# Optimization experiments

Hardware: AMD Instinct MI355X
Metric: run time of the kernel (lower is better)

## Reference

```python
import math
import jax, jax.numpy as jnp
import numpy as np

B, N, H, NH, DD, L = 4, 384, 256, 8, 32, 4
HD = H // NH
V = 11           # num_species + 1 (padding row 0)
CUTOFF = 5.0

def _ln(x, g, b):
    m = jnp.mean(x, axis=-1, keepdims=True)
    v = jnp.mean(jnp.square(x - m), axis=-1, keepdims=True)
    return (x - m) / jnp.sqrt(v + 1e-5) * g + b

def setup_inputs() -> dict:
    key = jax.random.key(0)
    ks = iter(jax.random.split(key, 64))
    def nrm(shape, s=0.05):
        return jax.random.normal(next(ks), shape, jnp.float32) * s
    return {
        'node_indices': jax.random.randint(next(ks), (B, N), 0, V),
        'positions': jax.random.normal(next(ks), (B, N, 3), jnp.float32),
        'mask': jnp.ones((B, N), jnp.float32),
        'emb': nrm((V, H)).at[0].set(0.0),
        'ln1_g': jnp.ones((L, H)), 'ln1_b': jnp.zeros((L, H)),
        'qkv_w': nrm((L, H, 3 * H)), 'qkv_b': jnp.zeros((L, 3 * H)),
        'out_w': nrm((L, H, H)), 'out_b': jnp.zeros((L, H)),
        'rb_w1': nrm((L, DD, H)), 'rb_b1': jnp.zeros((L, H)),
        'rb_w2': nrm((L, H, NH)), 'rb_b2': jnp.zeros((L, NH)),
        'gate_w1': nrm((L, H, H)), 'gate_b1': jnp.zeros((L, H)),
        'gate_w2': nrm((L, H, H)), 'gate_b2': jnp.zeros((L, H)),
        'ln2_g': jnp.ones((L, H)), 'ln2_b': jnp.zeros((L, H)),
        'ff_w1': nrm((L, H, 2 * H)), 'ff_b1': jnp.zeros((L, 2 * H)),
        'ff_w2': nrm((L, 2 * H, H)), 'ff_b2': jnp.zeros((L, H)),
        'pool_g': jnp.ones((H,)), 'pool_beta': jnp.zeros((H,)),
        'pool_w': nrm((H, H)), 'pool_b': jnp.zeros((H,)),
        'eh_w': nrm((H, 1)), 'eh_b': jnp.zeros((1,)),
    }

def _forward(node_indices, positions, mask, emb, ln1_g, ln1_b, qkv_w, qkv_b,
             out_w, out_b, rb_w1, rb_b1, rb_w2, rb_b2, gate_w1, gate_b1,
             gate_w2, gate_b2, ln2_g, ln2_b, ff_w1, ff_b1, ff_w2, ff_b2,
             pool_g, pool_beta, pool_w, pool_b, eh_w, eh_b):
    mask_b = mask > 0
    x = emb[node_indices] * mask_b[..., None]               # [B,N,H]
    pos = positions * mask_b[..., None].astype(positions.dtype)
    rel = pos[:, :, None, :] - pos[:, None, :, :]           # [B,N,N,3]
    dist = jnp.linalg.norm(rel + 1e-9, axis=-1)             # [B,N,N]
    adj = (dist <= CUTOFF).astype(jnp.float32)
    adj = adj * mask_b[:, None, :] * mask_b[:, :, None]
    edge = adj > 0
    isolated = mask_b & ~edge.any(axis=-1)
    adj = adj + isolated.astype(jnp.float32)[:, :, None] * jnp.eye(N, dtype=jnp.float32)
    edge = adj > 0
    # Bessel envelope features [B,N,N,DD]
    kk = jnp.arange(1, DD + 1, dtype=jnp.float32)
    ang = math.pi * kk * (dist / CUTOFF)[..., None]
    feat = jnp.sin(ang) / (dist[..., None] + 1e-6)
    feat = feat * (dist <= CUTOFF)[..., None].astype(jnp.float32)
    feat = feat * adj[..., None]

    scale = math.sqrt(HD)
    NEG = jnp.finfo(jnp.float32).min
    for l in range(L):
        res = x
        h = _ln(x, ln1_g[l], ln1_b[l])
        qkv = h @ qkv_w[l] + qkv_b[l]
        q, k, v = jnp.split(qkv, 3, axis=-1)
        q = q.reshape(B, N, NH, HD)
        k = k.reshape(B, N, NH, HD)
        v = v.reshape(B, N, NH, HD)
        logits = jnp.einsum('bihd,bjhd->bhij', q, k) / scale
        hb = jax.nn.silu(feat @ rb_w1[l] + rb_b1[l])        # [B,N,N,H]
        bias = hb @ rb_w2[l] + rb_b2[l]                     # [B,N,N,NH]
        logits = logits + bias.transpose(0, 3, 1, 2)
        logits = jnp.where(edge[:, None, :, :], logits, NEG)
        attn = jax.nn.softmax(logits, axis=-1)
        ctx = jnp.einsum('bhij,bjhd->bihd', attn, v).reshape(B, N, H)
        gated = jax.nn.silu(h @ gate_w1[l] + gate_b1[l]) @ gate_w2[l] + gate_b2[l]
        x = res + ((ctx * jax.nn.sigmoid(gated)) @ out_w[l] + out_b[l])
        y = _ln(x, ln2_g[l], ln2_b[l])
        x = x + (jax.nn.gelu(y @ ff_w1[l] + ff_b1[l], approximate=False) @ ff_w2[l] + ff_b2[l])

    pooled = jax.nn.silu(_ln(x, pool_g, pool_beta) @ pool_w + pool_b)
    masked = pooled * mask_b[..., None]
    counts = jnp.maximum(jnp.sum(mask_b, axis=1), 1)
    graph = jnp.sum(masked, axis=1) / counts[:, None]
    energy = (graph @ eh_w + eh_b)[:, 0]                    # [B]
    return energy

def reference(node_indices, positions, mask, emb, ln1_g, ln1_b, qkv_w, qkv_b,
              out_w, out_b, rb_w1, rb_b1, rb_w2, rb_b2, gate_w1, gate_b1,
              gate_w2, gate_b2, ln2_g, ln2_b, ff_w1, ff_b1, ff_w2, ff_b2,
              pool_g, pool_beta, pool_w, pool_b, eh_w, eh_b):
    return _forward(node_indices, positions, mask, emb, ln1_g, ln1_b, qkv_w,
                    qkv_b, out_w, out_b, rb_w1, rb_b1, rb_w2, rb_b2, gate_w1,
                    gate_b1, gate_w2, gate_b2, ln2_g, ln2_b, ff_w1, ff_b1,
                    ff_w2, ff_b2, pool_g, pool_beta, pool_w, pool_b, eh_w, eh_b)
```

## Files before the change

### kernel.cpp

```cpp
#include <hip/hip_runtime.h>
#include <hip/hip_bf16.h>
#include <math.h>

constexpr int B_ = 4, N_ = 384, H_ = 256, NH_ = 8, DD_ = 32, L_ = 4;
constexpr int M_ = B_ * N_;
constexpr float CUT = 5.0f;
constexpr float PI_ = 3.14159265358979323846f;
constexpr float INVSC = 0.17677669529663687f;
constexpr int TBL_N = 4096;
constexpr int TBL_STRIDE = 4098;

typedef __attribute__((ext_vector_type(8))) short short8;
typedef __attribute__((ext_vector_type(4))) float f32x4;
typedef __attribute__((ext_vector_type(4))) unsigned short u16x4;
using u16 = unsigned short;

__device__ __forceinline__ u16 f2b(float f) {
  __hip_bfloat16 h = __float2bfloat16(f);
  return *reinterpret_cast<u16*>(&h);
}
__device__ __forceinline__ float b2f(u16 u) {
  __hip_bfloat16 h;
  *reinterpret_cast<u16*>(&h) = u;
  return __bfloat162float(h);
}

__device__ __forceinline__ float wave_sum(float v) {
#pragma unroll
  for (int s = 1; s < 64; s <<= 1) v += __shfl_xor(v, s);
  return v;
}

__global__ __launch_bounds__(256) void embed_k(const int* __restrict__ idx,
                                               const float* __restrict__ mask,
                                               const float* __restrict__ emb,
                                               float* __restrict__ X) {
  int e = blockIdx.x * 256 + threadIdx.x;
  int mrow = e >> 8, c = e & 255;
  float mb = mask[mrow] > 0.f ? 1.f : 0.f;
  X[e] = emb[idx[mrow] * H_ + c] * mb;
}

__global__ __launch_bounds__(256) void dist_k(const float* __restrict__ pos,
                                              const float* __restrict__ mask,
                                              float* __restrict__ distm) {
  int e = blockIdx.x * 256 + threadIdx.x;
  int j = e % N_;
  int t = e / N_;
  int i = t % N_;
  int b = t / N_;
  float mi = mask[b * N_ + i], mj = mask[b * N_ + j];
  const float* pi = pos + (size_t)(b * N_ + i) * 3;
  const float* pj = pos + (size_t)(b * N_ + j) * 3;
  float dx = pi[0] - pj[0] + 1e-9f;
  float dy = pi[1] - pj[1] + 1e-9f;
  float dz = pi[2] - pj[2] + 1e-9f;
  float d = sqrtf(dx * dx + dy * dy + dz * dz);
  distm[e] = (mi > 0.f && mj > 0.f) ? d : 1e30f;
}

__global__ __launch_bounds__(256) void table_k(const float* __restrict__ rb_w1,
                                               const float* __restrict__ rb_b1,
                                               const float* __restrict__ rb_w2,
                                               const float* __restrict__ rb_b2,
                                               float* __restrict__ tbl2) {
  constexpr int TT = 64;
  int l = blockIdx.y;
  int t0 = blockIdx.x * TT;
  int tid = threadIdx.x;
  __shared__ float sfA[TT][32];
  __shared__ float hbA[TT][260];
#pragma unroll
  for (int m = 0; m < 8; m++) {
    int idx = m * 256 + tid;
    int tl = idx >> 5, k = idx & 31;
    int t = t0 + tl;
    float d = (t <= TBL_N) ? (t * (CUT / (float)TBL_N)) : 1.7320508075688772e-9f;
    float ang = PI_ * (k + 1) * d * (1.f / CUT);
    sfA[tl][k] = sinf(ang) / (d + 1e-6f);
  }
  __syncthreads();
  float w1c[32];
  const float* w1 = rb_w1 + (size_t)l * DD_ * H_;
#pragma unroll
  for (int k = 0; k < 32; k++) w1c[k] = w1[k * H_ + tid];
  float b1v = rb_b1[l * H_ + tid];
  for (int tl = 0; tl < TT; tl++) {
    float pre = b1v;
    const float4* sfp = (const float4*)sfA[tl];
#pragma unroll
    for (int kq = 0; kq < 8; kq++) {
      float4 s4 = sfp[kq];
      pre += s4.x * w1c[kq * 4] + s4.y * w1c[kq * 4 + 1] + s4.z * w1c[kq * 4 + 2] +
             s4.w * w1c[kq * 4 + 3];
    }
    hbA[tl][tid] = pre / (1.f + __expf(-pre));
  }
  __syncthreads();
  const float* w2 = rb_w2 + (size_t)l * H_ * NH_;
  int o = tid & 7;
  float b2v = rb_b2[l * NH_ + o];
#pragma unroll
  for (int half = 0; half < 2; half++) {
    int tl = (tid >> 3) + half * 32;
    float acc = b2v;
    const float4* hp = (const float4*)hbA[tl];
#pragma unroll 4
    for (int hq = 0; hq < 64; hq++) {
      float4 h4 = hp[hq];
      acc += h4.x * w2[(hq * 4 + 0) * NH_ + o] + h4.y * w2[(hq * 4 + 1) * NH_ + o] +
             h4.z * w2[(hq * 4 + 2) * NH_ + o] + h4.w * w2[(hq * 4 + 3) * NH_ + o];
    }
    int t = t0 + tl;
    if (t <= TBL_STRIDE) tbl2[(size_t)t * 32 + l * NH_ + o] = acc;
  }
}

__global__ __launch_bounds__(256) void bias_all2_k(const float* __restrict__ distm,
                                                   const float* __restrict__ tbl2,
                                                   u16* __restrict__ biasb) {
  int e = blockIdx.x * 256 + threadIdx.x;
  int j = e % N_;
  int t = e / N_;
  int i = t % N_;
  int b = t / N_;
  float d = distm[e];
  size_t plane = (size_t)N_ * N_;
  size_t obase = (size_t)b * NH_ * plane + (size_t)i * N_ + j;
  size_t lstride = (size_t)B_ * NH_ * plane;
  if (d <= CUT) {
    int ixrow;
    float fr;
    if (i == j) {
      ixrow = TBL_N + 1;
      fr = 0.f;
    } else {
      float u = d * ((float)TBL_N / CUT);
      int ix = (int)u;
      ix = ix > TBL_N - 1 ? TBL_N - 1 : ix;
      fr = u - (float)ix;
      ixrow = ix;
    }
    const float4* r0 = (const float4*)(tbl2 + (size_t)ixrow * 32);
    const float4* r1 = (const float4*)(tbl2 + (size_t)(ixrow + 1) * 32);
    float4 a0[8], a1[8];
#pragma unroll
    for (int q = 0; q < 8; q++) {
      a0[q] = r0[q];
      a1[q] = r1[q];
    }
    float w0 = 1.f - fr;
#pragma unroll
    for (int q = 0; q < 8; q++) {
      float v0[4] = {a0[q].x, a0[q].y, a0[q].z, a0[q].w};
      float v1[4] = {a1[q].x, a1[q].y, a1[q].z, a1[q].w};
#pragma unroll
      for (int c = 0; c < 4; c++) {
        int lh = q * 4 + c;
        int l = lh >> 3, h = lh & 7;
        float v = v0[c] * w0 + v1[c] * fr;
        biasb[(size_t)l * lstride + obase + (size_t)h * plane] = f2b(v);
      }
    }
  } else {
#pragma unroll
    for (int lh = 0; lh < 32; lh++) {
      int l = lh >> 3, h = lh & 7;
      biasb[(size_t)l * lstride + obase + (size_t)h * plane] = 0xFF80;
    }
  }
}

__global__ __launch_bounds__(256) void ln_k(const float* __restrict__ X,
                                            const float* __restrict__ g,
                                            const float* __restrict__ bta,
                                            u16* __restrict__ O) {
  int wave = threadIdx.x >> 6, lane = threadIdx.x & 63;
  int row = blockIdx.x * 4 + wave;
  const float* xr = X + (size_t)row * H_;
  float4 v = *(const float4*)(xr + lane * 4);
  float s = v.x + v.y + v.z + v.w;
  s = wave_sum(s);
  float m = s * (1.f / H_);
  float dx = v.x - m, dy = v.y - m, dz = v.z - m, dw = v.w - m;
  float vs = dx * dx + dy * dy + dz * dz + dw * dw;
  vs = wave_sum(vs);
  float rs = rsqrtf(vs * (1.f / H_) + 1e-5f);
  float4 gg = *(const float4*)(g + lane * 4);
  float4 bb = *(const float4*)(bta + lane * 4);
  u16x4 o;
  o[0] = f2b(dx * rs * gg.x + bb.x);
  o[1] = f2b(dy * rs * gg.y + bb.y);
  o[2] = f2b(dz * rs * gg.z + bb.z);
  o[3] = f2b(dw * rs * gg.w + bb.w);
  *(u16x4*)(O + (size_t)row * H_ + lane * 4) = o;
}

struct TrJob {
  const float* src;
  u16* dst;
  int K, N, nx, ny, nz, base, dstride;
};
struct TrJobs {
  TrJob j[7];
};
__global__ __launch_bounds__(256) void tr_all_k(TrJobs jobs) {
  __shared__ float t[32][33];
  int bid = blockIdx.x;
  int ji = 0;
#pragma unroll
  for (int q = 1; q < 7; q++)
    if (bid >= jobs.j[q].base) ji = q;
  const TrJob& J = jobs.j[ji];
  int local = bid - J.base;
  int z = local / (J.nx * J.ny);
  int r2 = local % (J.nx * J.ny);
  int ky = r2 / J.nx, kx = r2 % J.nx;
  int n0 = kx * 32, k0 = ky * 32;
  const float* s = J.src + (size_t)z * J.K * J.N;
  u16* d = J.dst + (size_t)z * J.dstride;
  int tid = threadIdx.x;
  int r = tid >> 3, c4 = (tid & 7) * 4;
  float4 v = *(const float4*)(s + (size_t)(k0 + r) * J.N + n0 + c4);
  t[r][c4 + 0] = v.x;
  t[r][c4 + 1] = v.y;
  t[r][c4 + 2] = v.z;
  t[r][c4 + 3] = v.w;
  __syncthreads();
  u16x4 o;
  o[0] = f2b(t[c4 + 0][r]);
  o[1] = f2b(t[c4 + 1][r]);
  o[2] = f2b(t[c4 + 2][r]);
  o[3] = f2b(t[c4 + 3][r]);
  *(u16x4*)(d + (size_t)(n0 + r) * J.K + k0 + c4) = o;
}

template <int ACT, bool RES, bool PRE, bool OBF>
__global__ __launch_bounds__(256) void mgemm_k(const void* __restrict__ Av,
                                               const u16* __restrict__ WT,
                                               const float* __restrict__ bias,
                                               const float* __restrict__ resid,
                                               void* __restrict__ Cv, int K, int Nc,
                                               int lda, const float* __restrict__ G,
                                               const float* __restrict__ bias2) {
  __shared__ u16 As[64 * 128];
  __shared__ u16 Bs[64 * 128];
  const int m0 = blockIdx.y * 64, n0 = blockIdx.x * 64;
  const int tid = threadIdx.x;
  const int wave = tid >> 6, lane = tid & 63;
  const int wr = wave >> 1, wc = wave & 1, lr = lane & 15, lg = lane >> 4;
  f32x4 acc[2][2] = {};
  const int srow = tid >> 2, sp = tid & 3;
  for (int k0 = 0; k0 < K; k0 += 128) {
#pragma unroll
    for (int s4 = 0; s4 < 4; s4++) {
      int s = sp * 4 + s4;
      int phys = s ^ (srow & 15);
      if (PRE) {
        const float* ap = (const float*)Av + (size_t)(m0 + srow) * lda + k0 + s * 8;
        const float* gp = G + (size_t)(m0 + srow) * lda + k0 + s * 8;
        float4 a0 = *(const float4*)ap;
        float4 a1 = *(const float4*)(ap + 4);
        float4 g0 = *(const float4*)gp;
        float4 g1 = *(const float4*)(gp + 4);
        short8 vv;
        vv[0] = (short)f2b(a0.x / (1.f + __expf(-g0.x)));
        vv[1] = (short)f2b(a0.y / (1.f + __expf(-g0.y)));
        vv[2] = (short)f2b(a0.z / (1.f + __expf(-g0.z)));
        vv[3] = (short)f2b(a0.w / (1.f + __expf(-g0.w)));
        vv[4] = (short)f2b(a1.x / (1.f + __expf(-g1.x)));
        vv[5] = (short)f2b(a1.y / (1.f + __expf(-g1.y)));
        vv[6] = (short)f2b(a1.z / (1.f + __expf(-g1.z)));
        vv[7] = (short)f2b(a1.w / (1.f + __expf(-g1.w)));
        *(short8*)&As[srow * 128 + phys * 8] = vv;
      } else {
        const u16* Ab = (const u16*)Av;
        short8 v = *(const short8*)(Ab + (size_t)(m0 + srow) * lda + k0 + s * 8);
        *(short8*)&As[srow * 128 + phys * 8] = v;
      }
      short8 w = *(const short8*)(WT + (size_t)(n0 + srow) * K + k0 + s * 8);
      *(short8*)&Bs[srow * 128 + phys * 8] = w;
    }
    __syncthreads();
#pragma unroll
    for (int kk = 0; kk < 4; kk++) {
      int slot = kk * 4 + lg;
      short8 af[2], bf_[2];
#pragma unroll
      for (int i = 0; i < 2; i++) {
        int row = wr * 32 + i * 16 + lr;
        af[i] = *(const short8*)&As[row * 128 + (slot ^ (row & 15)) * 8];
      }
#pragma unroll
      for (int j = 0; j < 2; j++) {
        int row = wc * 32 + j * 16 + lr;
        bf_[j] = *(const short8*)&Bs[row * 128 + (slot ^ (row & 15)) * 8];
      }
#pragma unroll
      for (int i = 0; i < 2; i++)
#pragma unroll
        for (int j = 0; j < 2; j++)
          acc[i][j] = __builtin_amdgcn_mfma_f32_16x16x32_bf16(af[i], bf_[j], acc[i][j], 0, 0, 0);
    }
    __syncthreads();
  }
#pragma unroll
  for (int i = 0; i < 2; i++)
#pragma unroll
    for (int j = 0; j < 2; j++)
#pragma unroll
      for (int rg = 0; rg < 4; rg++) {
        int row = m0 + wr * 32 + i * 16 + lg * 4 + rg;
        int col = n0 + wc * 32 + j * 16 + lr;
        float v;
        if (ACT == 3) {
          float bv = (col < 768) ? bias[col] : bias2[col - 768];
          v = acc[i][j][rg] + bv;
          if (col >= 768) v = v / (1.f + __expf(-v));
        } else {
          v = acc[i][j][rg] + bias[col];
          if (ACT == 1) v = v / (1.f + __expf(-v));
          if (ACT == 2) v = 0.5f * v * (1.f + erff(v * 0.70710678118654752f));
        }
        if (RES) v += resid[(size_t)row * Nc + col];
        if (OBF)
          ((u16*)Cv)[(size_t)row * Nc + col] = f2b(v);
        else
          ((float*)Cv)[(size_t)row * Nc + col] = v;
      }
}

__global__ __launch_bounds__(256) void attn_mf(const u16* __restrict__ qkv,
                                               const u16* __restrict__ biasb,
                                               float* __restrict__ ctx, int qs) {
  __shared__ __align__(16) u16 FragQ[2 * 64 * 8];
  __shared__ __align__(16) u16 FragK[24 * 64 * 8];
  __shared__ __align__(16) u16 FragV[24 * 64 * 8];
  __shared__ float smax[2][32];
  __shared__ float ssum[2][32];
  u16* FragP = FragK;
  float* pbuf = (float*)FragV;

  const int it = blockIdx.x, hh = blockIdx.y, b = blockIdx.z;
  const int i0 = it * 32;
  const int tid = threadIdx.x;
  const size_t bb = (size_t)b * N_;

  if (tid < 128) {
    int q = tid >> 2, dc = tid & 3;
    short8 v = *(const short8*)(qkv + (bb + i0 + q) * qs + hh * 32 + dc * 8);
    *(short8*)&FragQ[(((q >> 4) * 64) + (q & 15) + 16 * dc) * 8] = v;
  }
#pragma unroll
  for (int m = 0; m < 6; m++) {
    int idx = m * 256 + tid;
    int key = idx >> 2, dc = idx & 3;
    const u16* kb = qkv + (bb + key) * qs + 256 + hh * 32 + dc * 8;
    short8 kv = *(const short8*)kb;
    *(short8*)&FragK[(((key >> 4) * 64) + (key & 15) + 16 * dc) * 8] = kv;
    short8 vv = *(const short8*)(kb + 256);
    int kc = key >> 5, sub = (key >> 3) & 3, kj = key & 7;
#pragma unroll
    for (int j = 0; j < 8; j++) {
      int d = dc * 8 + j;
      FragV[(((kc * 2 + (d >> 4)) * 64) + (d & 15) + 16 * sub) * 8 + kj] = (u16)vv[j];
    }
  }
  __syncthreads();

  const int wave = tid >> 6, lane = tid & 63;
  const int rh = wave & 1, kh = wave >> 1;
  const int g = lane >> 4, c = lane & 15;
  const u16* bptr = biasb + (size_t)(b * NH_ + hh) * N_ * N_;

  short8 qf = *(const short8*)&FragQ[(rh * 64 + lane) * 8];
  f32x4 sc[12];
#pragma unroll
  for (int t = 0; t < 12; t++) {
    int T = kh * 12 + t;
    short8 kf = *(const short8*)&FragK[(T * 64 + lane) * 8];
    f32x4 z = {0.f, 0.f, 0.f, 0.f};
    sc[t] = __builtin_amdgcn_mfma_f32_16x16x32_bf16(qf, kf, z, 0, 0, 0);
    int key = 16 * T + c;
#pragma unroll
    for (int reg = 0; reg < 4; reg++) {
      int row = i0 + 16 * rh + 4 * g + reg;
      float bv = b2f(bptr[(size_t)row * N_ + key]);
      sc[t][reg] = sc[t][reg] * INVSC + bv;
    }
  }
  float mx[4];
#pragma unroll
  for (int reg = 0; reg < 4; reg++) {
    float m = sc[0][reg];
#pragma unroll
    for (int t = 1; t < 12; t++) m = fmaxf(m, sc[t][reg]);
#pragma unroll
    for (int s = 1; s < 16; s <<= 1) m = fmaxf(m, __shfl_xor(m, s));
    mx[reg] = m;
  }
  if (c == 0) {
#pragma unroll
    for (int reg = 0; reg < 4; reg++) smax[kh][16 * rh + 4 * g + reg] = mx[reg];
  }
  __syncthreads();
  float sm[4];
#pragma unroll
  for (int reg = 0; reg < 4; reg++) {
    float M = fmaxf(smax[0][16 * rh + 4 * g + reg], smax[1][16 * rh + 4 * g + reg]);
    float s = 0.f;
#pragma unroll
    for (int t = 0; t < 12; t++) {
      float p = __expf(sc[t][reg] - M);
      sc[t][reg] = p;
      s += p;
    }
    sm[reg] = s;
  }
#pragma unroll
  for (int reg = 0; reg < 4; reg++) {
#pragma unroll
    for (int s = 1; s < 16; s <<= 1) sm[reg] += __shfl_xor(sm[reg], s);
  }
  if (c == 0) {
#pragma unroll
    for (int reg = 0; reg < 4; reg++) ssum[kh][16 * rh + 4 * g + reg] = sm[reg];
  }
#pragma unroll
  for (int t = 0; t < 12; t++) {
    int T = kh * 12 + t;
    int kc = T >> 1;
    int sub = (2 * T + (c >> 3)) & 3;
#pragma unroll
    for (int reg = 0; reg < 4; reg++) {
      FragP[((rh * 12 + kc) * 64 + (4 * g + reg) + 16 * sub) * 8 + (c & 7)] =
          f2b(sc[t][reg]);
    }
  }
  __syncthreads();
  float Ls[4];
#pragma unroll
  for (int reg = 0; reg < 4; reg++)
    Ls[reg] = ssum[0][16 * rh + 4 * g + reg] + ssum[1][16 * rh + 4 * g + reg];

  f32x4 pcc[2] = {};
#pragma unroll
  for (int t = 0; t < 6; t++) {
    int kc = kh * 6 + t;
    short8 pf = *(const short8*)&FragP[((rh * 12 + kc) * 64 + lane) * 8];
#pragma unroll
    for (int nh = 0; nh < 2; nh++) {
      short8 vf = *(const short8*)&FragV[((kc * 2 + nh) * 64 + lane) * 8];
      pcc[nh] = __builtin_amdgcn_mfma_f32_16x16x32_bf16(pf, vf, pcc[nh], 0, 0, 0);
    }
  }
  __syncthreads();
  if (kh == 1) {
#pragma unroll
    for (int nh = 0; nh < 2; nh++)
#pragma unroll
      for (int reg = 0; reg < 4; reg++)
        pbuf[rh * 512 + (4 * g + reg) * 32 + nh * 16 + c] = pcc[nh][reg];
  }
  __syncthreads();
  if (kh == 0) {
#pragma unroll
    for (int nh = 0; nh < 2; nh++)
#pragma unroll
      for (int reg = 0; reg < 4; reg++) {
        float v = pcc[nh][reg] + pbuf[rh * 512 + (4 * g + reg) * 32 + nh * 16 + c];
        int row = i0 + 16 * rh + 4 * g + reg;
        ctx[(bb + row) * H_ + hh * 32 + nh * 16 + c] = v / Ls[reg];
      }
  }
}

__global__ __launch_bounds__(256) void energy_k(const float* __restrict__ p2,
                                                const float* __restrict__ mask,
                                                const float* __restrict__ ehw,
                                                const float* __restrict__ ehb,
                                                float* __restrict__ out) {
  int b = blockIdx.x, h = threadIdx.x;
  float s = 0.f, cnt = 0.f;
#pragma unroll 4
  for (int i = 0; i < N_; i++) {
    float m = mask[b * N_ + i] > 0.f ? 1.f : 0.f;
    s += p2[(size_t)(b * N_ + i) * H_ + h] * m;
    cnt += m;
  }
  float val = s * ehw[h];
  __shared__ float red[256];
  red[h] = val;
  __syncthreads();
  for (int st = 128; st > 0; st >>= 1) {
    if (h < st) red[h] += red[h + st];
    __syncthreads();
  }
  if (h == 0) {
    float c = cnt < 1.f ? 1.f : cnt;
    out[b] = red[0] / c + ehb[0];
  }
}

extern "C" void kernel_launch(void* const* d_in, const int* in_sizes, int n_in,
                              void* d_out, int out_size, void* d_ws, size_t ws_size,
                              hipStream_t stream) {
  const int* node_idx = (const int*)d_in[0];
  const float* positions = (const float*)d_in[1];
  const float* mask = (const float*)d_in[2];
  const float* emb = (const float*)d_in[3];
  const float* ln1_g = (const float*)d_in[4];
  const float* ln1_b = (const float*)d_in[5];
  const float* qkv_w = (const float*)d_in[6];
  const float* qkv_b = (const float*)d_in[7];
  const float* out_w = (const float*)d_in[8];
  const float* out_b = (const float*)d_in[9];
  const float* rb_w1 = (const float*)d_in[10];
  const float* rb_b1 = (const float*)d_in[11];
  const float* rb_w2 = (const float*)d_in[12];
  const float* rb_b2 = (const float*)d_in[13];
  const float* gate_w1 = (const float*)d_in[14];
  const float* gate_b1 = (const float*)d_in[15];
  const float* gate_w2 = (const float*)d_in[16];
  const float* gate_b2 = (const float*)d_in[17];
  const float* ln2_g = (const float*)d_in[18];
  const float* ln2_b = (const float*)d_in[19];
  const float* ff_w1 = (const float*)d_in[20];
  const float* ff_b1 = (const float*)d_in[21];
  const float* ff_w2 = (const float*)d_in[22];
  const float* ff_b2 = (const float*)d_in[23];
  const float* pool_g = (const float*)d_in[24];
  const float* pool_beta = (const float*)d_in[25];
  const float* pool_w = (const float*)d_in[26];
  const float* pool_b = (const float*)d_in[27];
  const float* eh_w = (const float*)d_in[28];
  const float* eh_b = (const float*)d_in[29];
  float* eout = (float*)d_out;

  char* W8 = (char*)d_ws;
  float* x = (float*)(W8 + 0);
  u16* qgb = (u16*)(W8 + 1572864);
  float* ctx = (float*)(W8 + 4718592);
  float* g2 = (float*)(W8 + 6291456);
  u16* hb = (u16*)(W8 + 7864320);
  u16* ffb = (u16*)(W8 + 8650752);
  float* distm = (float*)(W8 + 10223616);
  float* tbl2 = (float*)(W8 + 12582912);
  u16* wt = (u16*)(W8 + 13631488);
  u16* wt_qg = wt;
  u16* wt_out = wt + 1048576;
  u16* wt_g2 = wt + 1310720;
  u16* wt_f1 = wt + 1572864;
  u16* wt_f2 = wt + 2097152;
  u16* wt_p = wt + 2621440;
  u16* biasb = (u16*)(W8 + 19005440);
  const size_t bias_lstride = (size_t)B_ * NH_ * N_ * N_;

  embed_k<<<M_ * H_ / 256, 256, 0, stream>>>(node_idx, mask, emb, x);
  dist_k<<<B_ * N_ * N_ / 256, 256, 0, stream>>>(positions, mask, distm);
  table_k<<<dim3(65, L_), 256, 0, stream>>>(rb_w1, rb_b1, rb_w2, rb_b2, tbl2);
  {
    TrJobs jobs;
    jobs.j[0] = {qkv_w, wt_qg, 256, 768, 24, 8, 4, 0, 262144};
    jobs.j[1] = {gate_w1, wt_qg + 768 * 256, 256, 256, 8, 8, 4, 768, 262144};
    jobs.j[2] = {out_w, wt_out, 256, 256, 8, 8, 4, 1024, 65536};
    jobs.j[3] = {gate_w2, wt_g2, 256, 256, 8, 8, 4, 1280, 65536};
    jobs.j[4] = {ff_w1, wt_f1, 256, 512, 16, 8, 4, 1536, 131072};
    jobs.j[5] = {ff_w2, wt_f2, 512, 256, 8, 16, 4, 2048, 131072};
    jobs.j[6] = {pool_w, wt_p, 256, 256, 8, 8, 1, 2560, 65536};
    tr_all_k<<<2624, 256, 0, stream>>>(jobs);
  }
  bias_all2_k<<<B_ * N_ * N_ / 256, 256, 0, stream>>>(distm, tbl2, biasb);

  for (int l = 0; l < L_; l++) {
    const float* qb = qkv_b + (size_t)l * 3 * H_;
    const float* ob = out_b + (size_t)l * H_;
    const float* gb1 = gate_b1 + (size_t)l * H_;
    const float* gb2 = gate_b2 + (size_t)l * H_;
    const float* fb1 = ff_b1 + (size_t)l * 2 * H_;
    const float* fb2 = ff_b2 + (size_t)l * H_;
    u16* wqg = wt_qg + (size_t)l * 1024 * 256;
    u16* wo = wt_out + (size_t)l * 256 * 256;
    u16* wg2 = wt_g2 + (size_t)l * 256 * 256;
    u16* wf1 = wt_f1 + (size_t)l * 512 * 256;
    u16* wf2 = wt_f2 + (size_t)l * 256 * 512;

    ln_k<<<M_ / 4, 256, 0, stream>>>(x, ln1_g + l * H_, ln1_b + l * H_, hb);
    mgemm_k<3, false, false, true><<<dim3(16, 24), 256, 0, stream>>>(
        hb, wqg, qb, nullptr, qgb, 256, 1024, 256, nullptr, gb1);
    attn_mf<<<dim3(12, NH_, B_), 256, 0, stream>>>(
        qgb, biasb + (size_t)l * bias_lstride, ctx, 1024);
    mgemm_k<0, false, false, false><<<dim3(4, 24), 256, 0, stream>>>(
        (const void*)(qgb + 768), wg2, gb2, nullptr, g2, 256, 256, 1024, nullptr, nullptr);
    mgemm_k<0, true, true, false><<<dim3(4, 24), 256, 0, stream>>>(
        ctx, wo, ob, x, x, 256, 256, 256, g2, nullptr);
    ln_k<<<M_ / 4, 256, 0, stream>>>(x, ln2_g + l * H_, ln2_b + l * H_, hb);
    mgemm_k<2, false, false, true><<<dim3(8, 24), 256, 0, stream>>>(
        hb, wf1, fb1, nullptr, ffb, 256, 512, 256, nullptr, nullptr);
    mgemm_k<0, true, false, false><<<dim3(4, 24), 256, 0, stream>>>(
        ffb, wf2, fb2, x, x, 512, 256, 512, nullptr, nullptr);
  }

  ln_k<<<M_ / 4, 256, 0, stream>>>(x, pool_g, pool_beta, hb);
  mgemm_k<1, false, false, false><<<dim3(4, 24), 256, 0, stream>>>(
      hb, wt_p, pool_b, nullptr, ctx, 256, 256, 256, nullptr, nullptr);
  energy_k<<<B_, 256, 0, stream>>>(ctx, mask, eh_w, eh_b, eout);
}
```

Measured before the change: 307.9 us.

## Fuse LayerNorm into GEMM A-loads and distance computation into bias kernel

Result: slower. 366.7 us (+19.1%).

```diff
diff --git a/kernel.cpp b/kernel.cpp
--- a/kernel.cpp
+++ b/kernel.cpp
@@ -23,12 +23,6 @@
   __hip_bfloat16 h;
   *reinterpret_cast<u16*>(&h) = u;
   return __bfloat162float(h);
-}
-
-__device__ __forceinline__ float wave_sum(float v) {
-#pragma unroll
-  for (int s = 1; s < 64; s <<= 1) v += __shfl_xor(v, s);
-  return v;
 }
 
 __global__ __launch_bounds__(256) void embed_k(const int* __restrict__ idx,
@@ -41,9 +35,67 @@
   X[e] = emb[idx[mrow] * H_ + c] * mb;
 }
 
-__global__ __launch_bounds__(256) void dist_k(const float* __restrict__ pos,
-                                              const float* __restrict__ mask,
-                                              float* __restrict__ distm) {
+__global__ __launch_bounds__(256) void table_k(const float* __restrict__ rb_w1,
+                                               const float* __restrict__ rb_b1,
+                                               const float* __restrict__ rb_w2,
+                                               const float* __restrict__ rb_b2,
+                                               float* __restrict__ tbl2) {
+  constexpr int TT = 64;
+  int l = blockIdx.y;
+  int t0 = blockIdx.x * TT;
+  int tid = threadIdx.x;
+  __shared__ float sfA[TT][32];
+  __shared__ float hbA[TT][260];
+#pragma unroll
+  for (int m = 0; m < 8; m++) {
+    int idx = m * 256 + tid;
+    int tl = idx >> 5, k = idx & 31;
+    int t = t0 + tl;
+    float d = (t <= TBL_N) ? (t * (CUT / (float)TBL_N)) : 1.7320508075688772e-9f;
+    float ang = PI_ * (k + 1) * d * (1.f / CUT);
+    sfA[tl][k] = sinf(ang) / (d + 1e-6f);
+  }
+  __syncthreads();
+  float w1c[32];
+  const float* w1 = rb_w1 + (size_t)l * DD_ * H_;
+#pragma unroll
+  for (int k = 0; k < 32; k++) w1c[k] = w1[k * H_ + tid];
+  float b1v = rb_b1[l * H_ + tid];
+  for (int tl = 0; tl < TT; tl++) {
+    float pre = b1v;
+    const float4* sfp = (const float4*)sfA[tl];
+#pragma unroll
+    for (int kq = 0; kq < 8; kq++) {
+      float4 s4 = sfp[kq];
+      pre += s4.x * w1c[kq * 4] + s4.y * w1c[kq * 4 + 1] + s4.z * w1c[kq * 4 + 2] +
+             s4.w * w1c[kq * 4 + 3];
+    }
+    hbA[tl][tid] = pre / (1.f + __expf(-pre));
+  }
+  __syncthreads();
+  const float* w2 = rb_w2 + (size_t)l * H_ * NH_;
+  int o = tid & 7;
+  float b2v = rb_b2[l * NH_ + o];
+#pragma unroll
+  for (int half = 0; half < 2; half++) {
+    int tl = (tid >> 3) + half * 32;
+    float acc = b2v;
+    const float4* hp = (const float4*)hbA[tl];
+#pragma unroll 4
+    for (int hq = 0; hq < 64; hq++) {
+      float4 h4 = hp[hq];
+      acc += h4.x * w2[(hq * 4 + 0) * NH_ + o] + h4.y * w2[(hq * 4 + 1) * NH_ + o] +
+             h4.z * w2[(hq * 4 + 2) * NH_ + o] + h4.w * w2[(hq * 4 + 3) * NH_ + o];
+    }
+    int t = t0 + tl;
+    if (t <= TBL_STRIDE) tbl2[(size_t)t * 32 + l * NH_ + o] = acc;
+  }
+}
+
+__global__ __launch_bounds__(256) void bias_all2_k(const float* __restrict__ pos,
+                                                   const float* __restrict__ mask,
+                                                   const float* __restrict__ tbl2,
+                                                   u16* __restrict__ biasb) {
   int e = blockIdx.x * 256 + threadIdx.x;
   int j = e % N_;
   int t = e / N_;
@@ -56,79 +108,11 @@
   float dy = pi[1] - pj[1] + 1e-9f;
   float dz = pi[2] - pj[2] + 1e-9f;
   float d = sqrtf(dx * dx + dy * dy + dz * dz);
-  distm[e] = (mi > 0.f && mj > 0.f) ? d : 1e30f;
-}
-
-__global__ __launch_bounds__(256) void table_k(const float* __restrict__ rb_w1,
-                                               const float* __restrict__ rb_b1,
-                                               const float* __restrict__ rb_w2,
-                                               const float* __restrict__ rb_b2,
-                                               float* __restrict__ tbl2) {
-  constexpr int TT = 64;
-  int l = blockIdx.y;
-  int t0 = blockIdx.x * TT;
-  int tid = threadIdx.x;
-  __shared__ float sfA[TT][32];
-  __shared__ float hbA[TT][260];
-#pragma unroll
-  for (int m = 0; m < 8; m++) {
-    int idx = m * 256 + tid;
-    int tl = idx >> 5, k = idx & 31;
-    int t = t0 + tl;
-    float d = (t <= TBL_N) ? (t * (CUT / (float)TBL_N)) : 1.7320508075688772e-9f;
-    float ang = PI_ * (k + 1) * d * (1.f / CUT);
-    sfA[tl][k] = sinf(ang) / (d + 1e-6f);
-  }
-  __syncthreads();
-  float w1c[32];
-  const float* w1 = rb_w1 + (size_t)l * DD_ * H_;
-#pragma unroll
-  for (int k = 0; k < 32; k++) w1c[k] = w1[k * H_ + tid];
-  float b1v = rb_b1[l * H_ + tid];
-  for (int tl = 0; tl < TT; tl++) {
-    float pre = b1v;
-    const float4* sfp = (const float4*)sfA[tl];
-#pragma unroll
-    for (int kq = 0; kq < 8; kq++) {
-      float4 s4 = sfp[kq];
-      pre += s4.x * w1c[kq * 4] + s4.y * w1c[kq * 4 + 1] + s4.z * w1c[kq * 4 + 2] +
-             s4.w * w1c[kq * 4 + 3];
-    }
-    hbA[tl][tid] = pre / (1.f + __expf(-pre));
-  }
-  __syncthreads();
-  const float* w2 = rb_w2 + (size_t)l * H_ * NH_;
-  int o = tid & 7;
-  float b2v = rb_b2[l * NH_ + o];
-#pragma unroll
-  for (int half = 0; half < 2; half++) {
-    int tl = (tid >> 3) + half * 32;
-    float acc = b2v;
-    const float4* hp = (const float4*)hbA[tl];
-#pragma unroll 4
-    for (int hq = 0; hq < 64; hq++) {
-      float4 h4 = hp[hq];
-      acc += h4.x * w2[(hq * 4 + 0) * NH_ + o] + h4.y * w2[(hq * 4 + 1) * NH_ + o] +
-             h4.z * w2[(hq * 4 + 2) * NH_ + o] + h4.w * w2[(hq * 4 + 3) * NH_ + o];
-    }
-    int t = t0 + tl;
-    if (t <= TBL_STRIDE) tbl2[(size_t)t * 32 + l * NH_ + o] = acc;
-  }
-}
-
-__global__ __launch_bounds__(256) void bias_all2_k(const float* __restrict__ distm,
-                                                   const float* __restrict__ tbl2,
-                                                   u16* __restrict__ biasb) {
-  int e = blockIdx.x * 256 + threadIdx.x;
-  int j = e % N_;
-  int t = e / N_;
-  int i = t % N_;
-  int b = t / N_;
-  float d = distm[e];
+  bool edge = (mi > 0.f && mj > 0.f) && (d <= CUT);
   size_t plane = (size_t)N_ * N_;
   size_t obase = (size_t)b * NH_ * plane + (size_t)i * N_ + j;
   size_t lstride = (size_t)B_ * NH_ * plane;
-  if (d <= CUT) {
+  if (edge) {
     int ixrow;
     float fr;
     if (i == j) {
@@ -169,31 +153,6 @@
       biasb[(size_t)l * lstride + obase + (size_t)h * plane] = 0xFF80;
     }
   }
-}
-
-__global__ __launch_bounds__(256) void ln_k(const float* __restrict__ X,
-                                            const float* __restrict__ g,
-                                            const float* __restrict__ bta,
-                                            u16* __restrict__ O) {
-  int wave = threadIdx.x >> 6, lane = threadIdx.x & 63;
-  int row = blockIdx.x * 4 + wave;
-  const float* xr = X + (size_t)row * H_;
-  float4 v = *(const float4*)(xr + lane * 4);
-  float s = v.x + v.y + v.z + v.w;
-  s = wave_sum(s);
-  float m = s * (1.f / H_);
-  float dx = v.x - m, dy = v.y - m, dz = v.z - m, dw = v.w - m;
-  float vs = dx * dx + dy * dy + dz * dz + dw * dw;
-  vs = wave_sum(vs);
-  float rs = rsqrtf(vs * (1.f / H_) + 1e-5f);
-  float4 gg = *(const float4*)(g + lane * 4);
-  float4 bb = *(const float4*)(bta + lane * 4);
-  u16x4 o;
-  o[0] = f2b(dx * rs * gg.x + bb.x);
-  o[1] = f2b(dy * rs * gg.y + bb.y);
-  o[2] = f2b(dz * rs * gg.z + bb.z);
-  o[3] = f2b(dw * rs * gg.w + bb.w);
-  *(u16x4*)(O + (size_t)row * H_ + lane * 4) = o;
 }
 
 struct TrJob {
@@ -235,14 +194,16 @@
   *(u16x4*)(d + (size_t)(n0 + r) * J.K + k0 + c4) = o;
 }
 
-template <int ACT, bool RES, bool PRE, bool OBF>
+template <int ACT, bool RES, bool PRE, bool OBF, bool LNA>
 __global__ __launch_bounds__(256) void mgemm_k(const void* __restrict__ Av,
                                                const u16* __restrict__ WT,
                                                const float* __restrict__ bias,
                                                const float* __restrict__ resid,
                                                void* __restrict__ Cv, int K, int Nc,
                                                int lda, const float* __restrict__ G,
-                                               const float* __restrict__ bias2) {
+                                               const float* __restrict__ bias2,
+                                               const float* __restrict__ lng,
+                                               const float* __restrict__ lnb) {
   __shared__ u16 As[64 * 128];
   __shared__ u16 Bs[64 * 128];
   const int m0 = blockIdx.y * 64, n0 = blockIdx.x * 64;
@@ -251,27 +212,60 @@
   const int wr = wave >> 1, wc = wave & 1, lr = lane & 15, lg = lane >> 4;
   f32x4 acc[2][2] = {};
   const int srow = tid >> 2, sp = tid & 3;
+  float lnm = 0.f, lnrs = 0.f;
+  if (LNA) {
+    const float* xr = (const float*)Av + (size_t)(m0 + srow) * lda + sp * 64;
+    float s = 0.f, sq = 0.f;
+#pragma unroll
+    for (int i4 = 0; i4 < 16; i4++) {
+      float4 v = *(const float4*)(xr + i4 * 4);
+      s += v.x + v.y + v.z + v.w;
+      sq += v.x * v.x + v.y * v.y + v.z * v.z + v.w * v.w;
+    }
+    s += __shfl_xor(s, 1);
+    s += __shfl_xor(s, 2);
+    sq += __shfl_xor(sq, 1);
+    sq += __shfl_xor(sq, 2);
+    lnm = s * (1.f / 256.f);
+    lnrs = rsqrtf(sq * (1.f / 256.f) - lnm * lnm + 1e-5f);
+  }
   for (int k0 = 0; k0 < K; k0 += 128) {
 #pragma unroll
     for (int s4 = 0; s4 < 4; s4++) {
       int s = sp * 4 + s4;
       int phys = s ^ (srow & 15);
-      if (PRE) {
+      if (PRE || LNA) {
         const float* ap = (const float*)Av + (size_t)(m0 + srow) * lda + k0 + s * 8;
-        const float* gp = G + (size_t)(m0 + srow) * lda + k0 + s * 8;
         float4 a0 = *(const float4*)ap;
         float4 a1 = *(const float4*)(ap + 4);
-        float4 g0 = *(const float4*)gp;
-        float4 g1 = *(const float4*)(gp + 4);
         short8 vv;
-        vv[0] = (short)f2b(a0.x / (1.f + __expf(-g0.x)));
-        vv[1] = (short)f2b(a0.y / (1.f + __expf(-g0.y)));
-        vv[2] = (short)f2b(a0.z / (1.f + __expf(-g0.z)));
-        vv[3] = (short)f2b(a0.w / (1.f + __expf(-g0.w)));
-        vv[4] = (short)f2b(a1.x / (1.f + __expf(-g1.x)));
-        vv[5] = (short)f2b(a1.y / (1.f + __expf(-g1.y)));
-        vv[6] = (short)f2b(a1.z / (1.f + __expf(-g1.z)));
-        vv[7] = (short)f2b(a1.w / (1.f + __expf(-g1.w)));
+        if (PRE) {
+          const float* gp = G + (size_t)(m0 + srow) * lda + k0 + s * 8;
+          float4 g0 = *(const float4*)gp;
+          float4 g1 = *(const float4*)(gp + 4);
+          vv[0] = (short)f2b(a0.x / (1.f + __expf(-g0.x)));
+          vv[1] = (short)f2b(a0.y / (1.f + __expf(-g0.y)));
+          vv[2] = (short)f2b(a0.z / (1.f + __expf(-g0.z)));
+          vv[3] = (short)f2b(a0.w / (1.f + __expf(-g0.w)));
+          vv[4] = (short)f2b(a1.x / (1.f + __expf(-g1.x)));
+          vv[5] = (short)f2b(a1.y / (1.f + __expf(-g1.y)));
+          vv[6] = (short)f2b(a1.z / (1.f + __expf(-g1.z)));
+          vv[7] = (short)f2b(a1.w / (1.f + __expf(-g1.w)));
+        } else {
+          int c0 = k0 + s * 8;
+          float4 g0 = *(const float4*)(lng + c0);
+          float4 g1 = *(const float4*)(lng + c0 + 4);
+          float4 b0 = *(const float4*)(lnb + c0);
+          float4 b1 = *(const float4*)(lnb + c0 + 4);
+          vv[0] = (short)f2b((a0.x - lnm) * lnrs * g0.x + b0.x);
+          vv[1] = (short)f2b((a0.y - lnm) * lnrs * g0.y + b0.y);
+          vv[2] = (short)f2b((a0.z - lnm) * lnrs * g0.z + b0.z);
+          vv[3] = (short)f2b((a0.w - lnm) * lnrs * g0.w + b0.w);
+          vv[4] = (short)f2b((a1.x - lnm) * lnrs * g1.x + b1.x);
+          vv[5] = (short)f2b((a1.y - lnm) * lnrs * g1.y + b1.y);
+          vv[6] = (short)f2b((a1.z - lnm) * lnrs * g1.z + b1.z);
+          vv[7] = (short)f2b((a1.w - lnm) * lnrs * g1.w + b1.w);
+        }
         *(short8*)&As[srow * 128 + phys * 8] = vv;
       } else {
         const u16* Ab = (const u16*)Av;
@@ -542,9 +536,7 @@
   u16* qgb = (u16*)(W8 + 1572864);
   float* ctx = (float*)(W8 + 4718592);
   float* g2 = (float*)(W8 + 6291456);
-  u16* hb = (u16*)(W8 + 7864320);
   u16* ffb = (u16*)(W8 + 8650752);
-  float* distm = (float*)(W8 + 10223616);
   float* tbl2 = (float*)(W8 + 12582912);
   u16* wt = (u16*)(W8 + 13631488);
   u16* wt_qg = wt;
@@ -557,7 +549,6 @@
   const size_t bias_lstride = (size_t)B_ * NH_ * N_ * N_;
 
   embed_k<<<M_ * H_ / 256, 256, 0, stream>>>(node_idx, mask, emb, x);
-  dist_k<<<B_ * N_ * N_ / 256, 256, 0, stream>>>(positions, mask, distm);
   table_k<<<dim3(65, L_), 256, 0, stream>>>(rb_w1, rb_b1, rb_w2, rb_b2, tbl2);
   {
     TrJobs jobs;
@@ -570,7 +561,7 @@
     jobs.j[6] = {pool_w, wt_p, 256, 256, 8, 8, 1, 2560, 65536};
     tr_all_k<<<2624, 256, 0, stream>>>(jobs);
   }
-  bias_all2_k<<<B_ * N_ * N_ / 256, 256, 0, stream>>>(distm, tbl2, biasb);
+  bias_all2_k<<<B_ * N_ * N_ / 256, 256, 0, stream>>>(positions, mask, tbl2, biasb);
 
   for (int l = 0; l < L_; l++) {
     const float* qb = qkv_b + (size_t)l * 3 * H_;
@@ -585,24 +576,25 @@
     u16* wf1 = wt_f1 + (size_t)l * 512 * 256;
     u16* wf2 = wt_f2 + (size_t)l * 256 * 512;
 
-    ln_k<<<M_ / 4, 256, 0, stream>>>(x, ln1_g + l * H_, ln1_b + l * H_, hb);
-    mgemm_k<3, false, false, true><<<dim3(16, 24), 256, 0, stream>>>(
-        hb, wqg, qb, nullptr, qgb, 256, 1024, 256, nullptr, gb1);
+    mgemm_k<3, false, false, true, true><<<dim3(16, 24), 256, 0, stream>>>(
+        x, wqg, qb, nullptr, qgb, 256, 1024, 256, nullptr, gb1,
+        ln1_g + l * H_, ln1_b + l * H_);
     attn_mf<<<dim3(12, NH_, B_), 256, 0, stream>>>(
         qgb, biasb + (size_t)l * bias_lstride, ctx, 1024);
-    mgemm_k<0, false, false, false><<<dim3(4, 24), 256, 0, stream>>>(
-        (const void*)(qgb + 768), wg2, gb2, nullptr, g2, 256, 256, 1024, nullptr, nullptr);
-    mgemm_k<0, true, true, false><<<dim3(4, 24), 256, 0, stream>>>(
-        ctx, wo, ob, x, x, 256, 256, 256, g2, nullptr);
-    ln_k<<<M_ / 4, 256, 0, stream>>>(x, ln2_g + l * H_, ln2_b + l * H_, hb);
-    mgemm_k<2, false, false, true><<<dim3(8, 24), 256, 0, stream>>>(
-        hb, wf1, fb1, nullptr, ffb, 256, 512, 256, nullptr, nullptr);
-    mgemm_k<0, true, false, false><<<dim3(4, 24), 256, 0, stream>>>(
-        ffb, wf2, fb2, x, x, 512, 256, 512, nullptr, nullptr);
-  }
-
-  ln_k<<<M_ / 4, 256, 0, stream>>>(x, pool_g, pool_beta, hb);
-  mgemm_k<1, false, false, false><<<dim3(4, 24), 256, 0, stream>>>(
-      hb, wt_p, pool_b, nullptr, ctx, 256, 256, 256, nullptr, nullptr);
+    mgemm_k<0, false, false, false, false><<<dim3(4, 24), 256, 0, stream>>>(
+        (const void*)(qgb + 768), wg2, gb2, nullptr, g2, 256, 256, 1024,
+        nullptr, nullptr, nullptr, nullptr);
+    mgemm_k<0, true, true, false, false><<<dim3(4, 24), 256, 0, stream>>>(
+        ctx, wo, ob, x, x, 256, 256, 256, g2, nullptr, nullptr, nullptr);
+    mgemm_k<2, false, false, true, true><<<dim3(8, 24), 256, 0, stream>>>(
+        x, wf1, fb1, nullptr, ffb, 256, 512, 256, nullptr, nullptr,
+        ln2_g + l * H_, ln2_b + l * H_);
+    mgemm_k<0, true, false, false, false><<<dim3(4, 24), 256, 0, stream>>>(
+        ffb, wf2, fb2, x, x, 512, 256, 512, nullptr, nullptr, nullptr, nullptr);
+  }
+
+  mgemm_k<1, false, false, false, true><<<dim3(4, 24), 256, 0, stream>>>(
+      x, wt_p, pool_b, nullptr, ctx, 256, 256, 256, nullptr, nullptr,
+      pool_g, pool_beta);
   energy_k<<<B_, 256, 0, stream>>>(ctx, mask, eh_w, eh_b, eout);
 }
```

## Fuse distance into bias kernel and co-launch attention with gate GEMM

Applied to the files above, without the earlier changes.

Result: faster. 289.0 us (-6.1%).

```diff
diff --git a/kernel.cpp b/kernel.cpp
--- a/kernel.cpp
+++ b/kernel.cpp
@@ -41,9 +41,67 @@
   X[e] = emb[idx[mrow] * H_ + c] * mb;
 }
 
-__global__ __launch_bounds__(256) void dist_k(const float* __restrict__ pos,
-                                              const float* __restrict__ mask,
-                                              float* __restrict__ distm) {
+__global__ __launch_bounds__(256) void table_k(const float* __restrict__ rb_w1,
+                                               const float* __restrict__ rb_b1,
+                                               const float* __restrict__ rb_w2,
+                                               const float* __restrict__ rb_b2,
+                                               float* __restrict__ tbl2) {
+  constexpr int TT = 64;
+  int l = blockIdx.y;
+  int t0 = blockIdx.x * TT;
+  int tid = threadIdx.x;
+  __shared__ float sfA[TT][32];
+  __shared__ float hbA[TT][260];
+#pragma unroll
+  for (int m = 0; m < 8; m++) {
+    int idx = m * 256 + tid;
+    int tl = idx >> 5, k = idx & 31;
+    int t = t0 + tl;
+    float d = (t <= TBL_N) ? (t * (CUT / (float)TBL_N)) : 1.7320508075688772e-9f;
+    float ang = PI_ * (k + 1) * d * (1.f / CUT);
+    sfA[tl][k] = sinf(ang) / (d + 1e-6f);
+  }
+  __syncthreads();
+  float w1c[32];
+  const float* w1 = rb_w1 + (size_t)l * DD_ * H_;
+#pragma unroll
+  for (int k = 0; k < 32; k++) w1c[k] = w1[k * H_ + tid];
+  float b1v = rb_b1[l * H_ + tid];
+  for (int tl = 0; tl < TT; tl++) {
+    float pre = b1v;
+    const float4* sfp = (const float4*)sfA[tl];
+#pragma unroll
+    for (int kq = 0; kq < 8; kq++) {
+      float4 s4 = sfp[kq];
+      pre += s4.x * w1c[kq * 4] + s4.y * w1c[kq * 4 + 1] + s4.z * w1c[kq * 4 + 2] +
+             s4.w * w1c[kq * 4 + 3];
+    }
+    hbA[tl][tid] = pre / (1.f + __expf(-pre));
+  }
+  __syncthreads();
+  const float* w2 = rb_w2 + (size_t)l * H_ * NH_;
+  int o = tid & 7;
+  float b2v = rb_b2[l * NH_ + o];
+#pragma unroll
+  for (int half = 0; half < 2; half++) {
+    int tl = (tid >> 3) + half * 32;
+    float acc = b2v;
+    const float4* hp = (const float4*)hbA[tl];
+#pragma unroll 4
+    for (int hq = 0; hq < 64; hq++) {
+      float4 h4 = hp[hq];
+      acc += h4.x * w2[(hq * 4 + 0) * NH_ + o] + h4.y * w2[(hq * 4 + 1) * NH_ + o] +
+             h4.z * w2[(hq * 4 + 2) * NH_ + o] + h4.w * w2[(hq * 4 + 3) * NH_ + o];
+    }
+    int t = t0 + tl;
+    if (t <= TBL_STRIDE) tbl2[(size_t)t * 32 + l * NH_ + o] = acc;
+  }
+}
+
+__global__ __launch_bounds__(256) void bias_all2_k(const float* __restrict__ pos,
+                                                   const float* __restrict__ mask,
+                                                   const float* __restrict__ tbl2,
+                                                   u16* __restrict__ biasb) {
   int e = blockIdx.x * 256 + threadIdx.x;
   int j = e % N_;
   int t = e / N_;
@@ -56,79 +114,11 @@
   float dy = pi[1] - pj[1] + 1e-9f;
   float dz = pi[2] - pj[2] + 1e-9f;
   float d = sqrtf(dx * dx + dy * dy + dz * dz);
-  distm[e] = (mi > 0.f && mj > 0.f) ? d : 1e30f;
-}
-
-__global__ __launch_bounds__(256) void table_k(const float* __restrict__ rb_w1,
-                                               const float* __restrict__ rb_b1,
-                                               const float* __restrict__ rb_w2,
-                                               const float* __restrict__ rb_b2,
-                                               float* __restrict__ tbl2) {
-  constexpr int TT = 64;
-  int l = blockIdx.y;
-  int t0 = blockIdx.x * TT;
-  int tid = threadIdx.x;
-  __shared__ float sfA[TT][32];
-  __shared__ float hbA[TT][260];
-#pragma unroll
-  for (int m = 0; m < 8; m++) {
-    int idx = m * 256 + tid;
-    int tl = idx >> 5, k = idx & 31;
-    int t = t0 + tl;
-    float d = (t <= TBL_N) ? (t * (CUT / (float)TBL_N)) : 1.7320508075688772e-9f;
-    float ang = PI_ * (k + 1) * d * (1.f / CUT);
-    sfA[tl][k] = sinf(ang) / (d + 1e-6f);
-  }
-  __syncthreads();
-  float w1c[32];
-  const float* w1 = rb_w1 + (size_t)l * DD_ * H_;
-#pragma unroll
-  for (int k = 0; k < 32; k++) w1c[k] = w1[k * H_ + tid];
-  float b1v = rb_b1[l * H_ + tid];
-  for (int tl = 0; tl < TT; tl++) {
-    float pre = b1v;
-    const float4* sfp = (const float4*)sfA[tl];
-#pragma unroll
-    for (int kq = 0; kq < 8; kq++) {
-      float4 s4 = sfp[kq];
-      pre += s4.x * w1c[kq * 4] + s4.y * w1c[kq * 4 + 1] + s4.z * w1c[kq * 4 + 2] +
-             s4.w * w1c[kq * 4 + 3];
-    }
-    hbA[tl][tid] = pre / (1.f + __expf(-pre));
-  }
-  __syncthreads();
-  const float* w2 = rb_w2 + (size_t)l * H_ * NH_;
-  int o = tid & 7;
-  float b2v = rb_b2[l * NH_ + o];
-#pragma unroll
-  for (int half = 0; half < 2; half++) {
-    int tl = (tid >> 3) + half * 32;
-    float acc = b2v;
-    const float4* hp = (const float4*)hbA[tl];
-#pragma unroll 4
-    for (int hq = 0; hq < 64; hq++) {
-      float4 h4 = hp[hq];
-      acc += h4.x * w2[(hq * 4 + 0) * NH_ + o] + h4.y * w2[(hq * 4 + 1) * NH_ + o] +
-             h4.z * w2[(hq * 4 + 2) * NH_ + o] + h4.w * w2[(hq * 4 + 3) * NH_ + o];
-    }
-    int t = t0 + tl;
-    if (t <= TBL_STRIDE) tbl2[(size_t)t * 32 + l * NH_ + o] = acc;
-  }
-}
-
-__global__ __launch_bounds__(256) void bias_all2_k(const float* __restrict__ distm,
-                                                   const float* __restrict__ tbl2,
-                                                   u16* __restrict__ biasb) {
-  int e = blockIdx.x * 256 + threadIdx.x;
-  int j = e % N_;
-  int t = e / N_;
-  int i = t % N_;
-  int b = t / N_;
-  float d = distm[e];
+  bool edge = (mi > 0.f && mj > 0.f) && (d <= CUT);
   size_t plane = (size_t)N_ * N_;
   size_t obase = (size_t)b * NH_ * plane + (size_t)i * N_ + j;
   size_t lstride = (size_t)B_ * NH_ * plane;
-  if (d <= CUT) {
+  if (edge) {
     int ixrow;
     float fr;
     if (i == j) {
@@ -236,16 +226,15 @@
 }
 
 template <int ACT, bool RES, bool PRE, bool OBF>
-__global__ __launch_bounds__(256) void mgemm_k(const void* __restrict__ Av,
-                                               const u16* __restrict__ WT,
-                                               const float* __restrict__ bias,
-                                               const float* __restrict__ resid,
-                                               void* __restrict__ Cv, int K, int Nc,
-                                               int lda, const float* __restrict__ G,
-                                               const float* __restrict__ bias2) {
-  __shared__ u16 As[64 * 128];
-  __shared__ u16 Bs[64 * 128];
-  const int m0 = blockIdx.y * 64, n0 = blockIdx.x * 64;
+__device__ __forceinline__ void mgemm_body(u16* __restrict__ As, u16* __restrict__ Bs,
+                                           const void* __restrict__ Av,
+                                           const u16* __restrict__ WT,
+                                           const float* __restrict__ bias,
+                                           const float* __restrict__ resid,
+                                           void* __restrict__ Cv, int K, int Nc,
+                                           int lda, const float* __restrict__ G,
+                                           const float* __restrict__ bias2,
+                                           int m0, int n0) {
   const int tid = threadIdx.x;
   const int wave = tid >> 6, lane = tid & 63;
   const int wr = wave >> 1, wc = wave & 1, lr = lane & 15, lg = lane >> 4;
@@ -330,18 +319,29 @@
       }
 }
 
-__global__ __launch_bounds__(256) void attn_mf(const u16* __restrict__ qkv,
-                                               const u16* __restrict__ biasb,
-                                               float* __restrict__ ctx, int qs) {
-  __shared__ __align__(16) u16 FragQ[2 * 64 * 8];
-  __shared__ __align__(16) u16 FragK[24 * 64 * 8];
-  __shared__ __align__(16) u16 FragV[24 * 64 * 8];
-  __shared__ float smax[2][32];
-  __shared__ float ssum[2][32];
+template <int ACT, bool RES, bool PRE, bool OBF>
+__global__ __launch_bounds__(256) void mgemm_k(const void* __restrict__ Av,
+                                               const u16* __restrict__ WT,
+                                               const float* __restrict__ bias,
+                                               const float* __restrict__ resid,
+                                               void* __restrict__ Cv, int K, int Nc,
+                                               int lda, const float* __restrict__ G,
+                                               const float* __restrict__ bias2) {
+  __shared__ u16 As[64 * 128];
+  __shared__ u16 Bs[64 * 128];
+  mgemm_body<ACT, RES, PRE, OBF>(As, Bs, Av, WT, bias, resid, Cv, K, Nc, lda, G, bias2,
+                                 blockIdx.y * 64, blockIdx.x * 64);
+}
+
+__device__ __forceinline__ void attn_body(u16* __restrict__ FragQ, u16* __restrict__ FragK,
+                                          u16* __restrict__ FragV, float* __restrict__ smax,
+                                          float* __restrict__ ssum,
+                                          const u16* __restrict__ qkv,
+                                          const u16* __restrict__ biasb,
+                                          float* __restrict__ ctx, int qs,
+                                          int it, int hh, int b) {
   u16* FragP = FragK;
   float* pbuf = (float*)FragV;
-
-  const int it = blockIdx.x, hh = blockIdx.y, b = blockIdx.z;
   const int i0 = it * 32;
   const int tid = threadIdx.x;
   const size_t bb = (size_t)b * N_;
@@ -401,13 +401,13 @@
   }
   if (c == 0) {
 #pragma unroll
-    for (int reg = 0; reg < 4; reg++) smax[kh][16 * rh + 4 * g + reg] = mx[reg];
+    for (int reg = 0; reg < 4; reg++) smax[kh * 32 + 16 * rh + 4 * g + reg] = mx[reg];
   }
   __syncthreads();
   float sm[4];
 #pragma unroll
   for (int reg = 0; reg < 4; reg++) {
-    float M = fmaxf(smax[0][16 * rh + 4 * g + reg], smax[1][16 * rh + 4 * g + reg]);
+    float M = fmaxf(smax[16 * rh + 4 * g + reg], smax[32 + 16 * rh + 4 * g + reg]);
     float s = 0.f;
 #pragma unroll
     for (int t = 0; t < 12; t++) {
@@ -424,7 +424,7 @@
   }
   if (c == 0) {
 #pragma unroll
-    for (int reg = 0; reg < 4; reg++) ssum[kh][16 * rh + 4 * g + reg] = sm[reg];
+    for (int reg = 0; reg < 4; reg++) ssum[kh * 32 + 16 * rh + 4 * g + reg] = sm[reg];
   }
 #pragma unroll
   for (int t = 0; t < 12; t++) {
@@ -441,7 +441,7 @@
   float Ls[4];
 #pragma unroll
   for (int reg = 0; reg < 4; reg++)
-    Ls[reg] = ssum[0][16 * rh + 4 * g + reg] + ssum[1][16 * rh + 4 * g + reg];
+    Ls[reg] = ssum[16 * rh + 4 * g + reg] + ssum[32 + 16 * rh + 4 * g + reg];
 
   f32x4 pcc[2] = {};
 #pragma unroll
@@ -472,6 +472,28 @@
         int row = i0 + 16 * rh + 4 * g + reg;
         ctx[(bb + row) * H_ + hh * 32 + nh * 16 + c] = v / Ls[reg];
       }
+  }
+}
+
+__global__ __launch_bounds__(256) void attn_g2_k(const u16* __restrict__ qkv,
+                                                 const u16* __restrict__ biasb,
+                                                 float* __restrict__ ctx,
+                                                 const u16* __restrict__ wg2,
+                                                 const float* __restrict__ gb2,
+                                                 float* __restrict__ g2) {
+  __shared__ __align__(16) u16 SMEM[(2 + 24 + 24) * 64 * 8];
+  __shared__ float sred[2 * 32 * 2];
+  int bid = blockIdx.x;
+  if (bid < 384) {
+    int it = bid % 12;
+    int t = bid / 12;
+    attn_body(SMEM, SMEM + 1024, SMEM + 1024 + 12288, sred, sred + 64,
+              qkv, biasb, ctx, 1024, it, t % NH_, t / NH_);
+  } else {
+    int g = bid - 384;
+    mgemm_body<0, false, false, false>(SMEM, SMEM + 8192, (const void*)(qkv + 768), wg2,
+                                       gb2, nullptr, g2, 256, 256, 1024, nullptr,
+                                       nullptr, (g >> 2) * 64, (g & 3) * 64);
   }
 }
 
@@ -544,7 +566,6 @@
   float* g2 = (float*)(W8 + 6291456);
   u16* hb = (u16*)(W8 + 7864320);
   u16* ffb = (u16*)(W8 + 8650752);
-  float* distm = (float*)(W8 + 10223616);
   float* tbl2 = (float*)(W8 + 12582912);
   u16* wt = (u16*)(W8 + 13631488);
   u16* wt_qg = wt;
@@ -557,7 +578,6 @@
   const size_t bias_lstride = (size_t)B_ * NH_ * N_ * N_;
 
   embed_k<<<M_ * H_ / 256, 256, 0, stream>>>(node_idx, mask, emb, x);
-  dist_k<<<B_ * N_ * N_ / 256, 256, 0, stream>>>(positions, mask, distm);
   table_k<<<dim3(65, L_), 256, 0, stream>>>(rb_w1, rb_b1, rb_w2, rb_b2, tbl2);
   {
     TrJobs jobs;
@@ -570,7 +590,7 @@
     jobs.j[6] = {pool_w, wt_p, 256, 256, 8, 8, 1, 2560, 65536};
     tr_all_k<<<2624, 256, 0, stream>>>(jobs);
   }
-  bias_all2_k<<<B_ * N_ * N_ / 256, 256, 0, stream>>>(distm, tbl2, biasb);
+  bias_all2_k<<<B_ * N_ * N_ / 256, 256, 0, stream>>>(positions, mask, tbl2, biasb);
 
   for (int l = 0; l < L_; l++) {
     const float* qb = qkv_b + (size_t)l * 3 * H_;
@@ -588,10 +608,8 @@
     ln_k<<<M_ / 4, 256, 0, stream>>>(x, ln1_g + l * H_, ln1_b + l * H_, hb);
     mgemm_k<3, false, false, true><<<dim3(16, 24), 256, 0, stream>>>(
         hb, wqg, qb, nullptr, qgb, 256, 1024, 256, nullptr, gb1);
-    attn_mf<<<dim3(12, NH_, B_), 256, 0, stream>>>(
-        qgb, biasb + (size_t)l * bias_lstride, ctx, 1024);
-    mgemm_k<0, false, false, false><<<dim3(4, 24), 256, 0, stream>>>(
-        (const void*)(qgb + 768), wg2, gb2, nullptr, g2, 256, 256, 1024, nullptr, nullptr);
+    attn_g2_k<<<480, 256, 0, stream>>>(qgb, biasb + (size_t)l * bias_lstride, ctx,
+                                       wg2, gb2, g2);
     mgemm_k<0, true, true, false><<<dim3(4, 24), 256, 0, stream>>>(
         ctx, wo, ob, x, x, 256, 256, 256, g2, nullptr);
     ln_k<<<M_ / 4, 256, 0, stream>>>(x, ln2_g + l * H_, ln2_b + l * H_, hb);
```
